# Optimization experiments

Hardware: AMD Instinct MI355X
Metric: run time of the kernel (lower is better)

Reference implementation:

```python
import jax, jax.numpy as jnp
import numpy as np

B, N, DIM = 32, 131072, 64


def trilinear_sample(grid, pts):
    """Faithful F.grid_sample(mode='bilinear', padding_mode='zeros', align_corners=False).
    grid: [C, D, H, W]; pts: [B, N, 3] with (x, y, z) order: x->W, y->H, z->D.
    Returns [B, N, C]."""
    C, D, H, W = grid.shape
    # unnormalize, align_corners=False: ((c + 1) * size - 1) / 2
    ix = ((pts[..., 0] + 1.0) * W - 1.0) * 0.5
    iy = ((pts[..., 1] + 1.0) * H - 1.0) * 0.5
    iz = ((pts[..., 2] + 1.0) * D - 1.0) * 0.5
    x0f, y0f, z0f = jnp.floor(ix), jnp.floor(iy), jnp.floor(iz)
    tx, ty, tz = ix - x0f, iy - y0f, iz - z0f
    x0, y0, z0 = x0f.astype(jnp.int32), y0f.astype(jnp.int32), z0f.astype(jnp.int32)

    out = jnp.zeros((C,) + pts.shape[:-1], dtype=grid.dtype)  # [C, B, N]
    for dx in (0, 1):
        for dy in (0, 1):
            for dz in (0, 1):
                xc, yc, zc = x0 + dx, y0 + dy, z0 + dz
                w = (jnp.where(dx, tx, 1.0 - tx)
                     * jnp.where(dy, ty, 1.0 - ty)
                     * jnp.where(dz, tz, 1.0 - tz))
                valid = ((xc >= 0) & (xc < W) & (yc >= 0) & (yc < H)
                         & (zc >= 0) & (zc < D))
                xcc = jnp.clip(xc, 0, W - 1)
                ycc = jnp.clip(yc, 0, H - 1)
                zcc = jnp.clip(zc, 0, D - 1)
                v = grid[:, zcc, ycc, xcc]  # [C, B, N] gather
                out = out + v * (w * valid.astype(grid.dtype))[None]
    return jnp.moveaxis(out, 0, -1)  # [B, N, C]


def setup_inputs() -> dict:
    key = jax.random.key(0)
    k1, k2 = jax.random.split(key)
    x = jax.random.uniform(k1, (B, N, 3), dtype=jnp.float32, minval=-1.0, maxval=1.0)
    grid = 0.1 * jax.random.normal(k2, (3, DIM, DIM, DIM), dtype=jnp.float32)
    return {"x": x, "grid": grid}


def reference(x, grid):
    # x has 3 channels -> points == x; flow = grid_sample(grid, points); return x + flow
    flow = trilinear_sample(grid, x)  # [B, N, 3]
    return x + flow
```

## Files before the change

### kernel.cpp

```cpp
#include <hip/hip_runtime.h>

#define GD 64
#define GVOX (GD * GD * GD)

typedef float vfloat4 __attribute__((ext_vector_type(4)));
typedef int v4i __attribute__((ext_vector_type(4)));

__global__ __launch_bounds__(256) void repack_oct(const float* __restrict__ g,
                                                  v4i* __restrict__ pg) {
    int t = blockIdx.x * 256 + threadIdx.x;
    if (t >= GVOX) return;
    int x = t & 63, y = (t >> 6) & 63, z = t >> 12;
    int x1 = min(x + 1, GD - 1), y1 = min(y + 1, GD - 1), z1 = min(z + 1, GD - 1);

    float v[24];
#pragma unroll
    for (int dz = 0; dz < 2; ++dz)
#pragma unroll
        for (int dy = 0; dy < 2; ++dy)
#pragma unroll
            for (int dx = 0; dx < 2; ++dx) {
                int vox = ((dz ? z1 : z) << 12) | ((dy ? y1 : y) << 6) | (dx ? x1 : x);
                int c = dz * 4 + dy * 2 + dx;
#pragma unroll
                for (int ch = 0; ch < 3; ++ch) v[c * 3 + ch] = g[vox + ch * GVOX];
            }

    float vmax = 0.f;
#pragma unroll
    for (int k = 0; k < 24; ++k) vmax = fmaxf(vmax, fabsf(v[k]));

    int code = 0;
    float inv = 0.f;
    if (vmax > 0.f) {
        float s = vmax * (1.f / 15.f);
        int bits = __float_as_int(s);
        bits = (bits + 0x7FFFF) & ~0x7FFFF;
        int E = (bits >> 23) & 0xff;
        int m = (bits >> 19) & 0xf;
        int e = min(max(E - 107, 0), 15);
        code = (e << 4) | m;
        float sp = __int_as_float(((e + 107) << 23) | (m << 19));
        inv = 1.f / sp;
    }

    int dw[4] = {0, 0, 0, 0};
#pragma unroll
    for (int k = 0; k < 24; ++k) {
        int q = (int)rintf(v[k] * inv) + 15;
        q = min(max(q, 0), 30);
        dw[k / 6] |= q << (5 * (k % 6));
    }
    dw[0] |= (code & 3) << 30;
    dw[1] |= ((code >> 2) & 3) << 30;
    dw[2] |= ((code >> 4) & 3) << 30;
    dw[3] |= ((code >> 6) & 3) << 30;

    v4i o = {dw[0], dw[1], dw[2], dw[3]};
    pg[t] = o;
}

__device__ __forceinline__ void prep_point(float px, float py, float pz,
                                           int& idx, float* __restrict__ ew) {
    float ix = fmaf(px, 32.f, 31.5f);
    float iy = fmaf(py, 32.f, 31.5f);
    float iz = fmaf(pz, 32.f, 31.5f);
    float fx = floorf(ix), fy = floorf(iy), fz = floorf(iz);
    float tx = ix - fx, ty = iy - fy, tz = iz - fz;
    int x0 = (int)fx, y0 = (int)fy, z0 = (int)fz;

    ew[0] = (x0 < 0) ? tx : 1.f - tx;
    ew[1] = ((unsigned)x0 < 63u) ? tx : 0.f;
    ew[2] = (y0 < 0) ? ty : 1.f - ty;
    ew[3] = ((unsigned)y0 < 63u) ? ty : 0.f;
    ew[4] = (z0 < 0) ? tz : 1.f - tz;
    ew[5] = ((unsigned)z0 < 63u) ? tz : 0.f;

    int xc = min(max(x0, 0), GD - 1);
    int yc = min(max(y0, 0), GD - 1);
    int zc = min(max(z0, 0), GD - 1);
    idx = (zc << 12) | (yc << 6) | xc;
}

__device__ __forceinline__ void accum_oct(v4i r, const float* __restrict__ ew,
                                          float& o0, float& o1, float& o2) {
    int code = (int)(((unsigned)r[0] >> 30) | (((unsigned)r[1] >> 30) << 2) |
                     (((unsigned)r[2] >> 30) << 4) | (((unsigned)r[3] >> 30) << 6));
    float s = __int_as_float((((code >> 4) + 107) << 23) | ((code & 15) << 19));

    float sx0 = s * ew[0], sx1 = s * ew[1];
    float zy00 = ew[4] * ew[2], zy01 = ew[4] * ew[3];
    float zy10 = ew[5] * ew[2], zy11 = ew[5] * ew[3];
    float w[8] = {zy00 * sx0, zy00 * sx1, zy01 * sx0, zy01 * sx1,
                  zy10 * sx0, zy10 * sx1, zy11 * sx0, zy11 * sx1};

    float corr = -15.f * ((ew[4] + ew[5]) * (ew[2] + ew[3]) * (sx0 + sx1));
    float a0 = corr, a1 = corr, a2 = corr;
#pragma unroll
    for (int c = 0; c < 8; ++c) {
        unsigned dwv = (unsigned)r[c >> 1];
        int jb = 5 * ((c & 1) * 3);
        a0 = fmaf(w[c], (float)((dwv >> jb) & 31u), a0);
        a1 = fmaf(w[c], (float)((dwv >> (jb + 5)) & 31u), a1);
        a2 = fmaf(w[c], (float)((dwv >> (jb + 10)) & 31u), a2);
    }
    o0 += a0;
    o1 += a1;
    o2 += a2;
}

__device__ __forceinline__ void wave_lds_fence() {
    __builtin_amdgcn_wave_barrier();
    asm volatile("s_waitcnt lgkmcnt(0)" ::: "memory");
    __builtin_amdgcn_wave_barrier();
}

__global__ __launch_bounds__(64) void sample_oct(const vfloat4* __restrict__ pts,
                                                 const v4i* __restrict__ pg,
                                                 vfloat4* __restrict__ out,
                                                 int nf4) {
    __shared__ vfloat4 wbuf[192];
    int lane = threadIdx.x;
    int base = blockIdx.x * 192;

    bool full = (base + 192 <= nf4);

    vfloat4 v0 = {0.f, 0.f, 0.f, 0.f};
    vfloat4 v1 = {0.f, 0.f, 0.f, 0.f};
    vfloat4 v2 = {0.f, 0.f, 0.f, 0.f};
    if (full) {
        v0 = __builtin_nontemporal_load(&pts[base + lane]);
        v1 = __builtin_nontemporal_load(&pts[base + 64 + lane]);
        v2 = __builtin_nontemporal_load(&pts[base + 128 + lane]);
    } else {
        if (base + lane < nf4) v0 = __builtin_nontemporal_load(&pts[base + lane]);
        if (base + 64 + lane < nf4)
            v1 = __builtin_nontemporal_load(&pts[base + 64 + lane]);
        if (base + 128 + lane < nf4)
            v2 = __builtin_nontemporal_load(&pts[base + 128 + lane]);
    }
    wbuf[lane] = v0;
    wbuf[lane + 64] = v1;
    wbuf[lane + 128] = v2;
    wave_lds_fence();

    vfloat4 a = wbuf[lane * 3 + 0];
    vfloat4 b = wbuf[lane * 3 + 1];
    vfloat4 c = wbuf[lane * 3 + 2];
    float f[12] = {a.x, a.y, a.z, a.w, b.x, b.y, b.z, b.w, c.x, c.y, c.z, c.w};

    int idx[4];
    float ew[4][6];
#pragma unroll
    for (int p = 0; p < 4; ++p)
        prep_point(f[3 * p + 0], f[3 * p + 1], f[3 * p + 2], idx[p], ew[p]);

    v4i r[4];
#pragma unroll
    for (int p = 0; p < 4; ++p) r[p] = pg[idx[p]];

#pragma unroll
    for (int p = 0; p < 4; ++p)
        accum_oct(r[p], ew[p], f[3 * p + 0], f[3 * p + 1], f[3 * p + 2]);

    wbuf[lane * 3 + 0] = (vfloat4){f[0], f[1], f[2], f[3]};
    wbuf[lane * 3 + 1] = (vfloat4){f[4], f[5], f[6], f[7]};
    wbuf[lane * 3 + 2] = (vfloat4){f[8], f[9], f[10], f[11]};
    wave_lds_fence();

    if (full) {
        __builtin_nontemporal_store(wbuf[lane], &out[base + lane]);
        __builtin_nontemporal_store(wbuf[lane + 64], &out[base + 64 + lane]);
        __builtin_nontemporal_store(wbuf[lane + 128], &out[base + 128 + lane]);
    } else {
        if (base + lane < nf4)
            __builtin_nontemporal_store(wbuf[lane], &out[base + lane]);
        if (base + 64 + lane < nf4)
            __builtin_nontemporal_store(wbuf[lane + 64], &out[base + 64 + lane]);
        if (base + 128 + lane < nf4)
            __builtin_nontemporal_store(wbuf[lane + 128], &out[base + 128 + lane]);
    }
}

__device__ __forceinline__ void samp_add_direct(const float* __restrict__ g,
                                                float& px, float& py, float& pz) {
    float ix = fmaf(px, 32.f, 31.5f);
    float iy = fmaf(py, 32.f, 31.5f);
    float iz = fmaf(pz, 32.f, 31.5f);
    float fx = floorf(ix), fy = floorf(iy), fz = floorf(iz);
    float tx = ix - fx, ty = iy - fy, tz = iz - fz;
    int x0 = (int)fx, y0 = (int)fy, z0 = (int)fz;
    int xi0 = max(x0, 0), xi1 = min(x0 + 1, GD - 1);
    int yi0 = max(y0, 0), yi1 = min(y0 + 1, GD - 1);
    int zi0 = max(z0, 0), zi1 = min(z0 + 1, GD - 1);
    float wx0 = (1.f - tx) * (x0 >= 0 ? 1.f : 0.f);
    float wx1 = tx * (x0 < GD - 1 ? 1.f : 0.f);
    float wy0 = (1.f - ty) * (y0 >= 0 ? 1.f : 0.f);
    float wy1 = ty * (y0 < GD - 1 ? 1.f : 0.f);
    float wz0 = (1.f - tz) * (z0 >= 0 ? 1.f : 0.f);
    float wz1 = tz * (z0 < GD - 1 ? 1.f : 0.f);
    int zb0 = zi0 << 12, zb1 = zi1 << 12;
    int yb0 = yi0 << 6, yb1 = yi1 << 6;
    float wz0y0 = wz0 * wy0, wz0y1 = wz0 * wy1;
    float wz1y0 = wz1 * wy0, wz1y1 = wz1 * wy1;
    float s0 = 0.f, s1 = 0.f, s2 = 0.f;
#define CORNERD(zb, yb, xi, wgt)                 \
    {                                            \
        int idx = (zb) + (yb) + (xi);            \
        s0 = fmaf((wgt), g[idx], s0);            \
        s1 = fmaf((wgt), g[idx + GVOX], s1);     \
        s2 = fmaf((wgt), g[idx + 2 * GVOX], s2); \
    }
    CORNERD(zb0, yb0, xi0, wz0y0 * wx0);
    CORNERD(zb0, yb0, xi1, wz0y0 * wx1);
    CORNERD(zb0, yb1, xi0, wz0y1 * wx0);
    CORNERD(zb0, yb1, xi1, wz0y1 * wx1);
    CORNERD(zb1, yb0, xi0, wz1y0 * wx0);
    CORNERD(zb1, yb0, xi1, wz1y0 * wx1);
    CORNERD(zb1, yb1, xi0, wz1y1 * wx0);
    CORNERD(zb1, yb1, xi1, wz1y1 * wx1);
#undef CORNERD
    px += s0;
    py += s1;
    pz += s2;
}

__global__ __launch_bounds__(256) void sample_direct(const float* __restrict__ pts,
                                                     const float* __restrict__ g,
                                                     float* __restrict__ out, int npts) {
    int i = blockIdx.x * 256 + threadIdx.x;
    if (i >= npts) return;
    float x = pts[i * 3 + 0], y = pts[i * 3 + 1], z = pts[i * 3 + 2];
    samp_add_direct(g, x, y, z);
    out[i * 3 + 0] = x;
    out[i * 3 + 1] = y;
    out[i * 3 + 2] = z;
}

extern "C" void kernel_launch(void* const* d_in, const int* in_sizes, int n_in,
                              void* d_out, int out_size, void* d_ws, size_t ws_size,
                              hipStream_t stream) {
    const float* pts = (const float*)d_in[0];
    const float* grid = (const float*)d_in[1];

    int total_f = in_sizes[0];
    int npts = total_f / 3;

    if (ws_size >= (size_t)GVOX * 16 && (total_f % 4) == 0) {
        v4i* pg = (v4i*)d_ws;
        repack_oct<<<(GVOX + 255) / 256, 256, 0, stream>>>(grid, pg);
        int nf4 = total_f / 4;
        int nblocks = (nf4 + 191) / 192;
        sample_oct<<<nblocks, 64, 0, stream>>>((const vfloat4*)pts, pg,
                                               (vfloat4*)d_out, nf4);
    } else {
        sample_direct<<<(npts + 255) / 256, 256, 0, stream>>>(pts, grid,
                                                              (float*)d_out, npts);
    }
}
```

Baseline: 52.54 us.

## Convert sampler to persistent grid-stride loop with prefetch of next chunk

Replaces the one-chunk-per-block sampler with a persistent kernel capped at 4096 single-wave blocks that loops over chunks with a grid stride. The next chunk's point loads are issued after the grid gathers and before accumulation, so load latency can overlap with compute. This targets launch and scheduling overhead for many tiny blocks and exposed load latency. In exchange it holds more registers per wave and may reduce occupancy or latency hiding across waves.

```diff
diff --git a/kernel.cpp b/kernel.cpp
--- a/kernel.cpp
+++ b/kernel.cpp
@@ -115,70 +115,91 @@
     __builtin_amdgcn_wave_barrier();
 }
 
-__global__ __launch_bounds__(64) void sample_oct(const vfloat4* __restrict__ pts,
-                                                 const v4i* __restrict__ pg,
-                                                 vfloat4* __restrict__ out,
-                                                 int nf4) {
+__device__ __forceinline__ void load_chunk(const vfloat4* __restrict__ pts,
+                                           int base, int lane, int nf4,
+                                           vfloat4& r0, vfloat4& r1, vfloat4& r2) {
+    r0 = (vfloat4){0.f, 0.f, 0.f, 0.f};
+    r1 = r0;
+    r2 = r0;
+    if (base + 192 <= nf4) {
+        r0 = __builtin_nontemporal_load(&pts[base + lane]);
+        r1 = __builtin_nontemporal_load(&pts[base + 64 + lane]);
+        r2 = __builtin_nontemporal_load(&pts[base + 128 + lane]);
+    } else {
+        if (base + lane < nf4) r0 = __builtin_nontemporal_load(&pts[base + lane]);
+        if (base + 64 + lane < nf4)
+            r1 = __builtin_nontemporal_load(&pts[base + 64 + lane]);
+        if (base + 128 + lane < nf4)
+            r2 = __builtin_nontemporal_load(&pts[base + 128 + lane]);
+    }
+}
+
+__global__ __launch_bounds__(64) void sample_pipe(const vfloat4* __restrict__ pts,
+                                                  const v4i* __restrict__ pg,
+                                                  vfloat4* __restrict__ out,
+                                                  int nf4, int nchunks) {
     __shared__ vfloat4 wbuf[192];
     int lane = threadIdx.x;
-    int base = blockIdx.x * 192;
-
-    bool full = (base + 192 <= nf4);
-
-    vfloat4 v0 = {0.f, 0.f, 0.f, 0.f};
-    vfloat4 v1 = {0.f, 0.f, 0.f, 0.f};
-    vfloat4 v2 = {0.f, 0.f, 0.f, 0.f};
-    if (full) {
-        v0 = __builtin_nontemporal_load(&pts[base + lane]);
-        v1 = __builtin_nontemporal_load(&pts[base + 64 + lane]);
-        v2 = __builtin_nontemporal_load(&pts[base + 128 + lane]);
-    } else {
-        if (base + lane < nf4) v0 = __builtin_nontemporal_load(&pts[base + lane]);
-        if (base + 64 + lane < nf4)
-            v1 = __builtin_nontemporal_load(&pts[base + 64 + lane]);
-        if (base + 128 + lane < nf4)
-            v2 = __builtin_nontemporal_load(&pts[base + 128 + lane]);
-    }
-    wbuf[lane] = v0;
-    wbuf[lane + 64] = v1;
-    wbuf[lane + 128] = v2;
-    wave_lds_fence();
-
-    vfloat4 a = wbuf[lane * 3 + 0];
-    vfloat4 b = wbuf[lane * 3 + 1];
-    vfloat4 c = wbuf[lane * 3 + 2];
-    float f[12] = {a.x, a.y, a.z, a.w, b.x, b.y, b.z, b.w, c.x, c.y, c.z, c.w};
-
-    int idx[4];
-    float ew[4][6];
-#pragma unroll
-    for (int p = 0; p < 4; ++p)
-        prep_point(f[3 * p + 0], f[3 * p + 1], f[3 * p + 2], idx[p], ew[p]);
-
-    v4i r[4];
-#pragma unroll
-    for (int p = 0; p < 4; ++p) r[p] = pg[idx[p]];
-
-#pragma unroll
-    for (int p = 0; p < 4; ++p)
-        accum_oct(r[p], ew[p], f[3 * p + 0], f[3 * p + 1], f[3 * p + 2]);
-
-    wbuf[lane * 3 + 0] = (vfloat4){f[0], f[1], f[2], f[3]};
-    wbuf[lane * 3 + 1] = (vfloat4){f[4], f[5], f[6], f[7]};
-    wbuf[lane * 3 + 2] = (vfloat4){f[8], f[9], f[10], f[11]};
-    wave_lds_fence();
-
-    if (full) {
-        __builtin_nontemporal_store(wbuf[lane], &out[base + lane]);
-        __builtin_nontemporal_store(wbuf[lane + 64], &out[base + 64 + lane]);
-        __builtin_nontemporal_store(wbuf[lane + 128], &out[base + 128 + lane]);
-    } else {
-        if (base + lane < nf4)
+    int stride = gridDim.x;
+    int c = blockIdx.x;
+    if (c >= nchunks) return;
+
+    vfloat4 v0, v1, v2;
+    load_chunk(pts, c * 192, lane, nf4, v0, v1, v2);
+
+    while (true) {
+        int base = c * 192;
+        bool full = (base + 192 <= nf4);
+
+        wbuf[lane] = v0;
+        wbuf[lane + 64] = v1;
+        wbuf[lane + 128] = v2;
+        wave_lds_fence();
+
+        vfloat4 a = wbuf[lane * 3 + 0];
+        vfloat4 b = wbuf[lane * 3 + 1];
+        vfloat4 c3 = wbuf[lane * 3 + 2];
+        float f[12] = {a.x, a.y, a.z, a.w, b.x, b.y, b.z, b.w,
+                       c3.x, c3.y, c3.z, c3.w};
+
+        int idx[4];
+        float ew[4][6];
+#pragma unroll
+        for (int p = 0; p < 4; ++p)
+            prep_point(f[3 * p + 0], f[3 * p + 1], f[3 * p + 2], idx[p], ew[p]);
+
+        v4i r[4];
+#pragma unroll
+        for (int p = 0; p < 4; ++p) r[p] = pg[idx[p]];
+
+        int cn = c + stride;
+        bool has_next = (cn < nchunks);
+        if (has_next) load_chunk(pts, cn * 192, lane, nf4, v0, v1, v2);
+
+#pragma unroll
+        for (int p = 0; p < 4; ++p)
+            accum_oct(r[p], ew[p], f[3 * p + 0], f[3 * p + 1], f[3 * p + 2]);
+
+        wbuf[lane * 3 + 0] = (vfloat4){f[0], f[1], f[2], f[3]};
+        wbuf[lane * 3 + 1] = (vfloat4){f[4], f[5], f[6], f[7]};
+        wbuf[lane * 3 + 2] = (vfloat4){f[8], f[9], f[10], f[11]};
+        wave_lds_fence();
+
+        if (full) {
             __builtin_nontemporal_store(wbuf[lane], &out[base + lane]);
-        if (base + 64 + lane < nf4)
             __builtin_nontemporal_store(wbuf[lane + 64], &out[base + 64 + lane]);
-        if (base + 128 + lane < nf4)
             __builtin_nontemporal_store(wbuf[lane + 128], &out[base + 128 + lane]);
+        } else {
+            if (base + lane < nf4)
+                __builtin_nontemporal_store(wbuf[lane], &out[base + lane]);
+            if (base + 64 + lane < nf4)
+                __builtin_nontemporal_store(wbuf[lane + 64], &out[base + 64 + lane]);
+            if (base + 128 + lane < nf4)
+                __builtin_nontemporal_store(wbuf[lane + 128], &out[base + 128 + lane]);
+        }
+
+        if (!has_next) break;
+        c = cn;
     }
 }
 
@@ -250,9 +271,10 @@
         v4i* pg = (v4i*)d_ws;
         repack_oct<<<(GVOX + 255) / 256, 256, 0, stream>>>(grid, pg);
         int nf4 = total_f / 4;
-        int nblocks = (nf4 + 191) / 192;
-        sample_oct<<<nblocks, 64, 0, stream>>>((const vfloat4*)pts, pg,
-                                               (vfloat4*)d_out, nf4);
+        int nchunks = (nf4 + 191) / 192;
+        int nblocks = nchunks < 4096 ? nchunks : 4096;
+        sample_pipe<<<nblocks, 64, 0, stream>>>((const vfloat4*)pts, pg,
+                                                (vfloat4*)d_out, nf4, nchunks);
     } else {
         sample_direct<<<(npts + 255) / 256, 256, 0, stream>>>(pts, grid,
                                                               (float*)d_out, npts);
```

After: 53.77 us. 2.4% more time.
